# Kernel optimization log

Measured on AMD Instinct MI355X. Metric: run time of the kernel, lower is better.

The kernel has to match this reference:

```python
import jax, jax.numpy as jnp
import numpy as np

S = 128          # hidden mul for 0e and 1o in the GVP
M_OUT = 256      # 2*n_dets*el_emb_dim = 2*8*16
N_DETS = 8
FACTOR = 2 * N_DETS  # mul_to_axis factor = 16
EPS = 1e-8


def _gvp_layer(s, v, Wh, Wu, Wm, bm, activate):
    # s: (..., S) scalars (0e); v: (..., S, 3) vectors (1o)
    Vh = jnp.einsum('...mt,mh->...ht', v, Wh)                 # hidden vectors
    vn = jnp.sqrt(jnp.sum(Vh * Vh, axis=-1) + EPS)            # invariant norms
    sm = jnp.concatenate([s, vn], axis=-1) @ Wm + bm          # scalar channel
    Vu = jnp.einsum('...ht,ho->...ot', Vh, Wu)
    if activate:
        return jax.nn.silu(sm), Vu * jax.nn.sigmoid(sm)[..., None]
    return sm, Vu  # activate_final=False


def _gvp_mlp(x, params):
    s = x[..., :S]
    v = x[..., S:].reshape(x.shape[:-1] + (S, 3))
    n = len(params)
    for i, (Wh, Wu, Wm, bm) in enumerate(params):
        s, v = _gvp_layer(s, v, Wh, Wu, Wm, bm, activate=(i < n - 1))
    return s, v


def _anti_mlp(x, params):
    # antisymmetrize_e3_func: odd part under parity (1o components negated)
    s1, v1 = _gvp_mlp(x, params)
    xp = jnp.concatenate([x[..., :S], -x[..., S:]], axis=-1)
    s2, v2 = _gvp_mlp(xp, params)
    return 0.5 * (s1 - s2), 0.5 * (v1 - v2)


def setup_inputs() -> dict:
    key = jax.random.key(0)
    ks = jax.random.split(key, 11)
    B, NEL = 2048, 16
    f32 = jnp.float32
    inp = {
        'mo_coeffs': jax.random.normal(ks[0], (B, NEL, S * 4), dtype=f32),
        # GVP layer 0
        'Wh0': jax.random.normal(ks[1], (S, S), f32) / np.sqrt(S),
        'Wu0': jax.random.normal(ks[2], (S, S), f32) / np.sqrt(S),
        'Wm0': jax.random.normal(ks[3], (2 * S, S), f32) / np.sqrt(2 * S),
        'bm0': jnp.zeros((S,), f32),
        # GVP layer 1 (final, no activation)
        'Wh1': jax.random.normal(ks[4], (S, S), f32) / np.sqrt(S),
        'Wu1': jax.random.normal(ks[5], (S, S), f32) / np.sqrt(S),
        'Wm1': jax.random.normal(ks[6], (2 * S, S), f32) / np.sqrt(2 * S),
        'bm1': jnp.zeros((S,), f32),
        # NamedE3Linear: one weight per irrep block (0e and 1o)
        'W0': jax.random.normal(ks[7], (S, M_OUT), f32),
        'W1': jax.random.normal(ks[8], (S, M_OUT), f32),
    }
    return inp


def reference(mo_coeffs, Wh0, Wu0, Wm0, bm0, Wh1, Wu1, Wm1, bm1, W0, W1):
    params = [(Wh0, Wu0, Wm0, bm0), (Wh1, Wu1, Wm1, bm1)]
    s, v = _anti_mlp(mo_coeffs, params)           # (...,128), (...,128,3)
    inv_sqrt = 1.0 / np.sqrt(S).astype(np.float32)
    so = (s @ W0) * inv_sqrt                      # (..., 256)   0e block
    vo = jnp.einsum('...mt,mn->...nt', v, W1) * inv_sqrt  # (...,256,3) 1o block
    lead = so.shape[:-1]
    # mul_to_axis(16): mul 256 -> (16, 16); per-irrep flat dims concatenated
    so = so.reshape(lead + (FACTOR, M_OUT // FACTOR))            # (...,16,16)
    vo = vo.reshape(lead + (FACTOR, (M_OUT // FACTOR) * 3))      # (...,16,48)
    bf = jnp.concatenate([so, vo], axis=-1)                      # (...,16,64)
    # final reshape: (..., 2*n_dets, d) -> (..., 2, n_dets, d)
    bf = bf.reshape(lead + (2, N_DETS, bf.shape[-1]))
    return bf
```

## Files before the change

kernel.cpp:

```cpp
#include <hip/hip_runtime.h>
#include <hip/hip_bf16.h>


typedef __attribute__((ext_vector_type(8))) short short8;
typedef __attribute__((ext_vector_type(4))) float floatx4;

static __device__ __forceinline__ unsigned short f2bf(float f) {
  unsigned u = __float_as_uint(f);
  u = (u + 0x7fffu + ((u >> 16) & 1u)) >> 16;
  return (unsigned short)u;
}
static __device__ __forceinline__ unsigned pk2(float lo, float hi) {
  __hip_bfloat162 h = __float22bfloat162_rn(make_float2(lo, hi));
  return *(unsigned*)&h;
}

static __device__ __forceinline__ void put_sw(unsigned short* B, int k, int n,
                                              float val, int KT) {
  int kt = k >> 5, quad = (k >> 3) & 3, j = k & 7;
  int nt = n >> 4, c = n & 15;
  int lane = quad * 16 + c;
  B[(((nt * KT + kt) * 64 + lane) << 3) + j] = f2bf(val);
}

__global__ __launch_bounds__(128) void prep1(
    const float* __restrict__ Wh0, const float* __restrict__ Wu0,
    const float* __restrict__ Wh1, const float* __restrict__ Wu1,
    unsigned short* __restrict__ Wcat_sw, float* __restrict__ T) {
  int b = blockIdx.x, o = threadIdx.x;
  if (b < 128) {
    int m = b;
    float acc = 0.f;
    for (int h = 0; h < 128; ++h) acc += Wh0[m * 128 + h] * Wu0[h * 128 + o];
    put_sw(Wcat_sw, m, o, Wh0[m * 128 + o], 4);
    put_sw(Wcat_sw, m, o + 128, acc, 4);
  } else {
    int m = b - 128;
    float acc = 0.f;
    for (int h = 0; h < 128; ++h) acc += Wh1[m * 128 + h] * Wu1[h * 128 + o];
    T[m * 128 + o] = acc;
  }
}

__global__ __launch_bounds__(256) void prep2(
    const float* __restrict__ T, const float* __restrict__ W1,
    const float* __restrict__ Wm0, unsigned short* __restrict__ C_sw,
    unsigned short* __restrict__ Wm0_sw) {
  int b = blockIdx.x, tid = threadIdx.x;
  if (b < 128) {
    int m = b, n = tid;
    float acc = 0.f;
    for (int h = 0; h < 128; ++h) acc += T[m * 128 + h] * W1[h * 256 + n];
    put_sw(C_sw, m, n, acc * 0.08838834764831845f, 4);
  } else {
    int k = (b - 128) * 2 + (tid >> 7);
    int n = tid & 127;
    put_sw(Wm0_sw, k, n, Wm0[k * 128 + n], 8);
  }
}

#define XA_S 264
#define XV_S 136
#define XV_T 2176

__global__ __launch_bounds__(256, 4) void main_k(
    const float* __restrict__ x, const float* __restrict__ bm0,
    const unsigned short* __restrict__ Wcat_sw,
    const unsigned short* __restrict__ Wm0_sw,
    const unsigned short* __restrict__ C_sw, float* __restrict__ out) {
  __shared__ __align__(16) unsigned char smem[34560];
  unsigned short* v1 = (unsigned short*)smem;
  unsigned short* xa = (unsigned short*)(smem + 13056);
  unsigned short* xv = (unsigned short*)(smem + 21504);

  const int tid = threadIdx.x;
  const int lane = tid & 63;
  const int w = tid >> 6;
  const int l15 = lane & 15;
  const int quad = lane >> 4;
  const int r0 = blockIdx.x << 4;
  const float* xrow = x + (size_t)r0 * 512;
  const int ntg[4] = {2 * w, 2 * w + 1, 8 + 2 * w, 9 + 2 * w};

  float bias0 = bm0[(2 * w) * 16 + l15];
  float bias1 = bm0[(2 * w + 1) * 16 + l15];

#pragma unroll
  for (int i = 0; i < 2; ++i) {
    int e = tid + 256 * i;
    int r = e >> 5, c0 = (e & 31) << 2;
    float4 s4 = *(const float4*)(xrow + r * 512 + c0);
    uint2 p = make_uint2(pk2(s4.x, s4.y), pk2(s4.z, s4.w));
    *(uint2*)(xa + r * XA_S + c0) = p;
  }
#pragma unroll
  for (int i = 0; i < 2; ++i) {
    int e = tid + 256 * i;
    int r = e >> 5, mc = e & 31;
    const float* p = xrow + r * 512 + 128 + mc * 12;
    float4 a = *(const float4*)(p);
    float4 b = *(const float4*)(p + 4);
    float4 c = *(const float4*)(p + 8);
    float f[12] = {a.x, a.y, a.z, a.w, b.x, b.y, b.z, b.w, c.x, c.y, c.z, c.w};
#pragma unroll
    for (int t = 0; t < 3; ++t) {
      uint2 pk = make_uint2(pk2(f[t], f[t + 3]), pk2(f[t + 6], f[t + 9]));
      *(uint2*)(xv + t * XV_T + r * XV_S + mc * 4) = pk;
    }
  }
  __syncthreads();

  const floatx4 zf4 = {0.f, 0.f, 0.f, 0.f};

  floatx4 acc[3][4];
#pragma unroll
  for (int t = 0; t < 3; ++t)
#pragma unroll
    for (int j = 0; j < 4; ++j) acc[t][j] = zf4;
  for (int kt = 0; kt < 4; ++kt) {
    short8 bf[4];
#pragma unroll
    for (int j = 0; j < 4; ++j)
      bf[j] = *(const short8*)(Wcat_sw + (((ntg[j] * 4 + kt) * 64 + lane) << 3));
#pragma unroll
    for (int t = 0; t < 3; ++t) {
      short8 af = *(const short8*)(xv + t * XV_T + l15 * XV_S + kt * 32 + quad * 8);
#pragma unroll
      for (int j = 0; j < 4; ++j)
        acc[t][j] = __builtin_amdgcn_mfma_f32_16x16x32_bf16(af, bf[j], acc[t][j], 0, 0, 0);
    }
  }

#pragma unroll
  for (int j = 0; j < 2; ++j)
#pragma unroll
    for (int rg = 0; rg < 4; ++rg) {
      float s0 = acc[0][j][rg], s1 = acc[1][j][rg], s2 = acc[2][j][rg];
      float vn = sqrtf(s0 * s0 + s1 * s1 + s2 * s2 + 1e-8f);
      int r = quad * 4 + rg;
      int h = ntg[j] * 16 + l15;
      xa[r * XA_S + 128 + h] = f2bf(vn);
    }
  __syncthreads();

  floatx4 ga[2] = {zf4, zf4};
  for (int kt = 0; kt < 8; ++kt) {
    short8 af = *(const short8*)(xa + l15 * XA_S + kt * 32 + quad * 8);
    short8 b0 = *(const short8*)(Wm0_sw + ((((2 * w) * 8 + kt) * 64 + lane) << 3));
    short8 b1 = *(const short8*)(Wm0_sw + ((((2 * w + 1) * 8 + kt) * 64 + lane) << 3));
    ga[0] = __builtin_amdgcn_mfma_f32_16x16x32_bf16(af, b0, ga[0], 0, 0, 0);
    ga[1] = __builtin_amdgcn_mfma_f32_16x16x32_bf16(af, b1, ga[1], 0, 0, 0);
  }
  float g[2][4];
#pragma unroll
  for (int j = 0; j < 2; ++j) {
    float bias = j ? bias1 : bias0;
#pragma unroll
    for (int rg = 0; rg < 4; ++rg)
      g[j][rg] = 1.f / (1.f + __expf(-(ga[j][rg] + bias)));
  }
#pragma unroll
  for (int t = 0; t < 3; ++t)
#pragma unroll
    for (int j = 0; j < 2; ++j)
#pragma unroll
      for (int rg = 0; rg < 4; ++rg) {
        int r = quad * 4 + rg;
        int o = (2 * w + j) * 16 + l15;
        v1[t * XV_T + r * XV_S + o] = f2bf(acc[t][2 + j][rg] * g[j][rg]);
      }
  __syncthreads();

  floatx4 vacc[3][4];
#pragma unroll
  for (int t = 0; t < 3; ++t)
#pragma unroll
    for (int j = 0; j < 4; ++j) vacc[t][j] = zf4;
  for (int kt = 0; kt < 4; ++kt) {
    short8 bf[4];
#pragma unroll
    for (int j = 0; j < 4; ++j)
      bf[j] = *(const short8*)(C_sw + (((ntg[j] * 4 + kt) * 64 + lane) << 3));
#pragma unroll
    for (int t = 0; t < 3; ++t) {
      short8 af = *(const short8*)(v1 + t * XV_T + l15 * XV_S + kt * 32 + quad * 8);
#pragma unroll
      for (int j = 0; j < 4; ++j)
        vacc[t][j] = __builtin_amdgcn_mfma_f32_16x16x32_bf16(af, bf[j], vacc[t][j], 0, 0, 0);
    }
  }

  float* orow = out + (size_t)r0 * 1024;
#pragma unroll
  for (int i = 0; i < 4; ++i) {
    int e = tid + 256 * i;
    int r = e >> 6, gblk = (e >> 2) & 15, s4 = e & 3;
    *(float4*)(orow + (size_t)r * 1024 + gblk * 64 + s4 * 4) =
        make_float4(0.f, 0.f, 0.f, 0.f);
  }
#pragma unroll
  for (int j = 0; j < 4; ++j) {
    int nt = ntg[j];
#pragma unroll
    for (int rg = 0; rg < 4; ++rg) {
      int r = quad * 4 + rg;
      *(float3*)(orow + (size_t)r * 1024 + nt * 64 + 16 + 3 * l15) =
          make_float3(vacc[0][j][rg], vacc[1][j][rg], vacc[2][j][rg]);
    }
  }
}

extern "C" void kernel_launch(void* const* d_in, const int* in_sizes, int n_in,
                              void* d_out, int out_size, void* d_ws,
                              size_t ws_size, hipStream_t stream) {
  const float* mo = (const float*)d_in[0];
  const float* Wh0 = (const float*)d_in[1];
  const float* Wu0 = (const float*)d_in[2];
  const float* Wm0 = (const float*)d_in[3];
  const float* bm0 = (const float*)d_in[4];
  const float* Wh1 = (const float*)d_in[5];
  const float* Wu1 = (const float*)d_in[6];
  const float* W1 = (const float*)d_in[10];

  unsigned short* ws = (unsigned short*)d_ws;
  unsigned short* Wcat_sw = ws;
  unsigned short* C_sw = ws + 32768;
  unsigned short* Wm0_sw = ws + 65536;
  float* T = (float*)(ws + 98304);

  prep1<<<256, 128, 0, stream>>>(Wh0, Wu0, Wh1, Wu1, Wcat_sw, T);
  prep2<<<256, 256, 0, stream>>>(T, W1, Wm0, C_sw, Wm0_sw);

  main_k<<<2048, 256, 0, stream>>>(mo, bm0, Wcat_sw, Wm0_sw, C_sw,
                                   (float*)d_out);
}
```

Before: 224.5 us.

## Merge prep kernels, alias v1 onto xv to cut LDS, and raise occupancy

Fuses the two weight-prep kernels into one launch, keeping the Wh1·Wu1 row in shared memory so the intermediate T buffer disappears. The main kernel reuses the xv region for v1, cutting shared memory from about 34.5KB to 21.5KB, and raises launch bounds to 5 waves per SIMD. The Wm0 GEMM is split so its first half (original scalars) runs before the barrier that publishes the norm values. Output zero-fill moves to the start of the kernel. The aliasing relies on the barrier ordering xv reads before v1 writes, and the tighter register budget could cause spills.

```diff
diff --git a/kernel.cpp b/kernel.cpp
--- a/kernel.cpp
+++ b/kernel.cpp
@@ -23,39 +23,38 @@
   B[(((nt * KT + kt) * 64 + lane) << 3) + j] = f2bf(val);
 }
 
-__global__ __launch_bounds__(128) void prep1(
+__global__ __launch_bounds__(128) void prep(
     const float* __restrict__ Wh0, const float* __restrict__ Wu0,
     const float* __restrict__ Wh1, const float* __restrict__ Wu1,
-    unsigned short* __restrict__ Wcat_sw, float* __restrict__ T) {
-  int b = blockIdx.x, o = threadIdx.x;
+    const float* __restrict__ W1, const float* __restrict__ Wm0,
+    unsigned short* __restrict__ Wcat_sw, unsigned short* __restrict__ C_sw,
+    unsigned short* __restrict__ Wm0_sw) {
+  __shared__ float trow[128];
+  int b = blockIdx.x, tid = threadIdx.x;
   if (b < 128) {
-    int m = b;
+    int m = b, o = tid;
     float acc = 0.f;
     for (int h = 0; h < 128; ++h) acc += Wh0[m * 128 + h] * Wu0[h * 128 + o];
     put_sw(Wcat_sw, m, o, Wh0[m * 128 + o], 4);
     put_sw(Wcat_sw, m, o + 128, acc, 4);
+  } else if (b < 256) {
+    int m = b - 128, o = tid;
+    float acc = 0.f;
+    for (int p = 0; p < 128; ++p) acc += Wh1[m * 128 + p] * Wu1[p * 128 + o];
+    trow[o] = acc;
+    __syncthreads();
+#pragma unroll
+    for (int nn = 0; nn < 2; ++nn) {
+      int n = tid + 128 * nn;
+      float c = 0.f;
+      for (int h = 0; h < 128; ++h) c += trow[h] * W1[h * 256 + n];
+      put_sw(C_sw, m, n, c * 0.08838834764831845f, 4);
+    }
   } else {
-    int m = b - 128;
-    float acc = 0.f;
-    for (int h = 0; h < 128; ++h) acc += Wh1[m * 128 + h] * Wu1[h * 128 + o];
-    T[m * 128 + o] = acc;
-  }
-}
-
-__global__ __launch_bounds__(256) void prep2(
-    const float* __restrict__ T, const float* __restrict__ W1,
-    const float* __restrict__ Wm0, unsigned short* __restrict__ C_sw,
-    unsigned short* __restrict__ Wm0_sw) {
-  int b = blockIdx.x, tid = threadIdx.x;
-  if (b < 128) {
-    int m = b, n = tid;
-    float acc = 0.f;
-    for (int h = 0; h < 128; ++h) acc += T[m * 128 + h] * W1[h * 256 + n];
-    put_sw(C_sw, m, n, acc * 0.08838834764831845f, 4);
-  } else {
-    int k = (b - 128) * 2 + (tid >> 7);
-    int n = tid & 127;
-    put_sw(Wm0_sw, k, n, Wm0[k * 128 + n], 8);
+    int kb = (b - 256) * 8;
+#pragma unroll
+    for (int kk = 0; kk < 8; ++kk)
+      put_sw(Wm0_sw, kb + kk, tid, Wm0[(kb + kk) * 128 + tid], 8);
   }
 }
 
@@ -63,15 +62,15 @@
 #define XV_S 136
 #define XV_T 2176
 
-__global__ __launch_bounds__(256, 4) void main_k(
+__global__ __launch_bounds__(256, 5) void main_k(
     const float* __restrict__ x, const float* __restrict__ bm0,
     const unsigned short* __restrict__ Wcat_sw,
     const unsigned short* __restrict__ Wm0_sw,
     const unsigned short* __restrict__ C_sw, float* __restrict__ out) {
-  __shared__ __align__(16) unsigned char smem[34560];
-  unsigned short* v1 = (unsigned short*)smem;
-  unsigned short* xa = (unsigned short*)(smem + 13056);
-  unsigned short* xv = (unsigned short*)(smem + 21504);
+  __shared__ __align__(16) unsigned char smem[21504];
+  unsigned short* xa = (unsigned short*)smem;
+  unsigned short* xv = (unsigned short*)(smem + 8448);
+  unsigned short* v1 = xv;
 
   const int tid = threadIdx.x;
   const int lane = tid & 63;
@@ -80,7 +79,16 @@
   const int quad = lane >> 4;
   const int r0 = blockIdx.x << 4;
   const float* xrow = x + (size_t)r0 * 512;
+  float* orow = out + (size_t)r0 * 1024;
   const int ntg[4] = {2 * w, 2 * w + 1, 8 + 2 * w, 9 + 2 * w};
+
+#pragma unroll
+  for (int i = 0; i < 4; ++i) {
+    int e = tid + 256 * i;
+    int r = e >> 6, gblk = (e >> 2) & 15, s4 = e & 3;
+    *(float4*)(orow + (size_t)r * 1024 + gblk * 64 + s4 * 4) =
+        make_float4(0.f, 0.f, 0.f, 0.f);
+  }
 
   float bias0 = bm0[(2 * w) * 16 + l15];
   float bias1 = bm0[(2 * w + 1) * 16 + l15];
@@ -90,8 +98,7 @@
     int e = tid + 256 * i;
     int r = e >> 5, c0 = (e & 31) << 2;
     float4 s4 = *(const float4*)(xrow + r * 512 + c0);
-    uint2 p = make_uint2(pk2(s4.x, s4.y), pk2(s4.z, s4.w));
-    *(uint2*)(xa + r * XA_S + c0) = p;
+    *(uint2*)(xa + r * XA_S + c0) = make_uint2(pk2(s4.x, s4.y), pk2(s4.z, s4.w));
   }
 #pragma unroll
   for (int i = 0; i < 2; ++i) {
@@ -103,10 +110,9 @@
     float4 c = *(const float4*)(p + 8);
     float f[12] = {a.x, a.y, a.z, a.w, b.x, b.y, b.z, b.w, c.x, c.y, c.z, c.w};
 #pragma unroll
-    for (int t = 0; t < 3; ++t) {
-      uint2 pk = make_uint2(pk2(f[t], f[t + 3]), pk2(f[t + 6], f[t + 9]));
-      *(uint2*)(xv + t * XV_T + r * XV_S + mc * 4) = pk;
-    }
+    for (int t = 0; t < 3; ++t)
+      *(uint2*)(xv + t * XV_T + r * XV_S + mc * 4) =
+          make_uint2(pk2(f[t], f[t + 3]), pk2(f[t + 6], f[t + 9]));
   }
   __syncthreads();
 
@@ -137,20 +143,27 @@
     for (int rg = 0; rg < 4; ++rg) {
       float s0 = acc[0][j][rg], s1 = acc[1][j][rg], s2 = acc[2][j][rg];
       float vn = sqrtf(s0 * s0 + s1 * s1 + s2 * s2 + 1e-8f);
-      int r = quad * 4 + rg;
-      int h = ntg[j] * 16 + l15;
-      xa[r * XA_S + 128 + h] = f2bf(vn);
-    }
-  __syncthreads();
+      xa[(quad * 4 + rg) * XA_S + 128 + ntg[j] * 16 + l15] = f2bf(vn);
+    }
 
   floatx4 ga[2] = {zf4, zf4};
-  for (int kt = 0; kt < 8; ++kt) {
+  for (int kt = 0; kt < 4; ++kt) {
     short8 af = *(const short8*)(xa + l15 * XA_S + kt * 32 + quad * 8);
     short8 b0 = *(const short8*)(Wm0_sw + ((((2 * w) * 8 + kt) * 64 + lane) << 3));
     short8 b1 = *(const short8*)(Wm0_sw + ((((2 * w + 1) * 8 + kt) * 64 + lane) << 3));
     ga[0] = __builtin_amdgcn_mfma_f32_16x16x32_bf16(af, b0, ga[0], 0, 0, 0);
     ga[1] = __builtin_amdgcn_mfma_f32_16x16x32_bf16(af, b1, ga[1], 0, 0, 0);
   }
+  __syncthreads();
+
+  for (int kt = 4; kt < 8; ++kt) {
+    short8 af = *(const short8*)(xa + l15 * XA_S + kt * 32 + quad * 8);
+    short8 b0 = *(const short8*)(Wm0_sw + ((((2 * w) * 8 + kt) * 64 + lane) << 3));
+    short8 b1 = *(const short8*)(Wm0_sw + ((((2 * w + 1) * 8 + kt) * 64 + lane) << 3));
+    ga[0] = __builtin_amdgcn_mfma_f32_16x16x32_bf16(af, b0, ga[0], 0, 0, 0);
+    ga[1] = __builtin_amdgcn_mfma_f32_16x16x32_bf16(af, b1, ga[1], 0, 0, 0);
+  }
+
   float g[2][4];
 #pragma unroll
   for (int j = 0; j < 2; ++j) {
@@ -164,11 +177,9 @@
 #pragma unroll
     for (int j = 0; j < 2; ++j)
 #pragma unroll
-      for (int rg = 0; rg < 4; ++rg) {
-        int r = quad * 4 + rg;
-        int o = (2 * w + j) * 16 + l15;
-        v1[t * XV_T + r * XV_S + o] = f2bf(acc[t][2 + j][rg] * g[j][rg]);
-      }
+      for (int rg = 0; rg < 4; ++rg)
+        v1[t * XV_T + (quad * 4 + rg) * XV_S + (2 * w + j) * 16 + l15] =
+            f2bf(acc[t][2 + j][rg] * g[j][rg]);
   __syncthreads();
 
   floatx4 vacc[3][4];
@@ -190,14 +201,6 @@
     }
   }
 
-  float* orow = out + (size_t)r0 * 1024;
-#pragma unroll
-  for (int i = 0; i < 4; ++i) {
-    int e = tid + 256 * i;
-    int r = e >> 6, gblk = (e >> 2) & 15, s4 = e & 3;
-    *(float4*)(orow + (size_t)r * 1024 + gblk * 64 + s4 * 4) =
-        make_float4(0.f, 0.f, 0.f, 0.f);
-  }
 #pragma unroll
   for (int j = 0; j < 4; ++j) {
     int nt = ntg[j];
@@ -226,11 +229,9 @@
   unsigned short* Wcat_sw = ws;
   unsigned short* C_sw = ws + 32768;
   unsigned short* Wm0_sw = ws + 65536;
-  float* T = (float*)(ws + 98304);
-
-  prep1<<<256, 128, 0, stream>>>(Wh0, Wu0, Wh1, Wu1, Wcat_sw, T);
-  prep2<<<256, 256, 0, stream>>>(T, W1, Wm0, C_sw, Wm0_sw);
-
+
+  prep<<<288, 128, 0, stream>>>(Wh0, Wu0, Wh1, Wu1, W1, Wm0, Wcat_sw, C_sw,
+                                Wm0_sw);
   main_k<<<2048, 256, 0, stream>>>(mo, bm0, Wcat_sw, Wm0_sw, C_sw,
                                    (float*)d_out);
 }
```

Measured after the change: 249.1 us. +11.0%, slower.
